# Kernel tuning notes

Hardware: AMD Instinct MI355X
Metric: run time of the kernel (lower is better)

Reference implementation:

```python
import jax, jax.numpy as jnp
import numpy as np
from jax import lax

H = 16  # hidden size

def lstm_dir(x_tbd, Wih, Whh, bih, bhh):
    # x_tbd: [T, B, D] -> outputs [T, B, H], final h [B, H]
    T, B, _ = x_tbd.shape
    xg = jnp.einsum('tbd,gd->tbg', x_tbd, Wih) + bih + bhh  # [T, B, 4H]
    def step(carry, xt):
        h, c = carry
        g = xt + h @ Whh.T
        i, f, gg, o = jnp.split(g, 4, axis=-1)  # PyTorch gate order i,f,g,o
        i = jax.nn.sigmoid(i); f = jax.nn.sigmoid(f)
        gg = jnp.tanh(gg); o = jax.nn.sigmoid(o)
        c = f * c + i * gg
        h = o * jnp.tanh(c)
        return (h, c), h
    init = (jnp.zeros((B, H), x_tbd.dtype), jnp.zeros((B, H), x_tbd.dtype))
    (hT, cT), hs = lax.scan(step, init, xg)
    return hs, hT

def bi_layer(x_tbd, pf, pb):
    hs_f, hT_f = lstm_dir(x_tbd, *pf)
    hs_b_rev, hT_b = lstm_dir(x_tbd[::-1], *pb)
    out = jnp.concatenate([hs_f, hs_b_rev[::-1]], axis=-1)  # [T, B, 2H]
    return out, hT_f, hT_b


def setup_inputs() -> dict:
    key = jax.random.key(0)
    ks = iter(jax.random.split(key, 32))
    B, T = 4096, 512
    d = {"x": jax.random.normal(next(ks), (B, T), jnp.float32)}
    def w(shape):
        return jax.random.normal(next(ks), shape, jnp.float32) * 0.2
    # layer 0 (input dim 1), forward / backward directions
    for s in ('f', 'b'):
        d[f'Wih0{s}'] = w((4 * H, 1)); d[f'Whh0{s}'] = w((4 * H, H))
        d[f'bih0{s}'] = jnp.zeros((4 * H,), jnp.float32)
        d[f'bhh0{s}'] = jnp.zeros((4 * H,), jnp.float32)
    # layer 1 (input dim 2H = 32)
    for s in ('f', 'b'):
        d[f'Wih1{s}'] = w((4 * H, 2 * H)); d[f'Whh1{s}'] = w((4 * H, H))
        d[f'bih1{s}'] = jnp.zeros((4 * H,), jnp.float32)
        d[f'bhh1{s}'] = jnp.zeros((4 * H,), jnp.float32)
    # MLP head: Linear(32,25), Linear(25,20)
    d['W1'] = w((25, 2 * H)); d['b1'] = jnp.zeros((25,), jnp.float32)
    d['W2'] = w((20, 25)); d['b2'] = jnp.zeros((20,), jnp.float32)
    return d


def reference(x, Wih0f, Whh0f, bih0f, bhh0f, Wih0b, Whh0b, bih0b, bhh0b,
              Wih1f, Whh1f, bih1f, bhh1f, Wih1b, Whh1b, bih1b, bhh1b,
              W1, b1, W2, b2):
    # x: [B, T] -> unsqueeze(2) -> [B, T, 1]; scan over time, so transpose to [T, B, 1]
    x_tbd = x.T[:, :, None]
    o0, _, _ = bi_layer(x_tbd, (Wih0f, Whh0f, bih0f, bhh0f), (Wih0b, Whh0b, bih0b, bhh0b))
    # dropout=0.1 between layers is inactive in eval mode (reference = eval)
    _, hT_f, hT_b = bi_layer(o0, (Wih1f, Whh1f, bih1f, bhh1f), (Wih1b, Whh1b, bih1b, bhh1b))
    # torch: cat((h[-1], h[-2]), 1) = (last-layer backward, last-layer forward)
    feat = jnp.concatenate([hT_b, hT_f], axis=1)  # [B, 32]
    z = jax.nn.elu(feat)
    z = jax.nn.elu(z @ W1.T + b1)
    z = jax.nn.elu(z @ W2.T + b2)
    return z  # [B, 20]
```

## Files before the change

### kernel.cpp

```cpp
#include <hip/hip_runtime.h>
#include <stdint.h>

#define TT 512
#define BB 4096
#define NT8 512
#define LOG2E 1.4426950408889634f

typedef _Float16 half8_t __attribute__((ext_vector_type(8)));
typedef __fp16 fp16x2_t __attribute__((ext_vector_type(2)));
typedef float f32x4 __attribute__((ext_vector_type(4)));
typedef float f32x2 __attribute__((ext_vector_type(2)));

union FragU { uint4 u4; half8_t h8; };
union PkU { fp16x2_t h2; unsigned int u; };

__device__ __forceinline__ float rcp_(float x){ return __builtin_amdgcn_rcpf(x); }
__device__ __forceinline__ float exp2_(float x){ return __builtin_amdgcn_exp2f(x); }
__device__ __forceinline__ float elu_(float x){ return x > 0.0f ? x : (exp2_(x * LOG2E) - 1.0f); }
__device__ __forceinline__ int mini_(int a, int b){ return a < b ? a : b; }
__device__ __forceinline__ float maskhi_(float x){ return __uint_as_float(__float_as_uint(x) & 0xFFFFE000u); }
__device__ __forceinline__ unsigned int pkrtz_(float a, float b){
    PkU p; p.h2 = __builtin_amdgcn_cvt_pkrtz(a, b); return p.u;
}
__device__ __forceinline__ unsigned int pkrne_(float a, float b){
    PkU p; p.h2[0] = (__fp16)a; p.h2[1] = (__fp16)b; return p.u;
}

__device__ __forceinline__ f32x4 MFMA(half8_t a, half8_t b, f32x4 c) {
    return __builtin_amdgcn_mfma_f32_16x16x32_f16(a, b, c, 0, 0, 0);
}

__device__ __forceinline__ f32x4 ld4_(const float* p){ return *(const f32x4*)p; }

__device__ __forceinline__ half8_t packA8s(const float* s, float sc) {
    half8_t h;
#pragma unroll
    for (int k = 0; k < 8; ++k) h[k] = (_Float16)(s[k] * sc);
    return h;
}
__device__ __forceinline__ half8_t zero8_() {
    half8_t h;
#pragma unroll
    for (int k = 0; k < 8; ++k) h[k] = (_Float16)0.0f;
    return h;
}

__device__ __forceinline__ void cell2p_(f32x2 gi, f32x2 gf, f32x2 gg, f32x2 go,
                                        f32x2& c, f32x2& h) {
    f32x2 ei, ef, eg, eo;
    ei[0] = exp2_(-gi[0]); ei[1] = exp2_(-gi[1]);
    ef[0] = exp2_(-gf[0]); ef[1] = exp2_(-gf[1]);
    eg[0] = exp2_(-gg[0]); eg[1] = exp2_(-gg[1]);
    eo[0] = exp2_(-go[0]); eo[1] = exp2_(-go[1]);
    const f32x2 one = {1.0f, 1.0f};
    f32x2 ai = one + ei, af = one + ef, ag = one + eg, ao = one + eo;
    f32x2 pif = ai * af, pgo = ag * ao;
    f32x2 P = pif * pgo;
    f32x2 R; R[0] = rcp_(P[0]); R[1] = rcp_(P[1]);
    f32x2 I = R * (af * pgo);
    f32x2 F = R * (ai * pgo);
    f32x2 Gt = R * (pif * ao);
    f32x2 O = R * (pif * ag);
    f32x2 G = Gt + Gt - one;
    c = F * c + I * G;
    f32x2 ct = c * (-2.0f * LOG2E);
    f32x2 et; et[0] = exp2_(ct[0]); et[1] = exp2_(ct[1]);
    f32x2 den = one + et;
    f32x2 Rt; Rt[0] = rcp_(den[0]); Rt[1] = rcp_(den[1]);
    f32x2 T = Rt + Rt - one;
    h = O * T;
}


struct PA {
    const float *x;
    const float *WihF, *WhhF, *bihF, *bhhF;
    const float *WihB, *WhhB, *bihB, *bhhB;
    char* ws;
};

__global__ __launch_bounds__(256) void phaseA_k(PA p) {
    const int tid = threadIdx.x;
    const int lane = tid & 63;
    const int wv   = tid >> 6;
    const int q = lane >> 4, b = lane & 15, c = b & 7;
    const bool hi8 = b >= 8;
    const int chain = blockIdx.x * 4 + wv;
    const int tile = chain >> 1, dir = chain & 1;

    const float* Wih = dir ? p.WihB : p.WihF;
    const float* Whh = dir ? p.WhhB : p.WhhF;
    const float* bih = dir ? p.bihB : p.bihF;
    const float* bhh = dir ? p.bhhB : p.bhhF;

    auto mkA = [&](int m, float sc)->half8_t {
        if (q < 2) return packA8s(Whh + (16*m + b)*16 + 8*q, sc);
        half8_t h = zero8_();
        if (q == 2) {
            float w = Wih[16*m + b] * sc;
            h[0] = (_Float16)w;
            h[1] = (_Float16)w;
        }
        return h;
    };
    half8_t A0 = mkA(0, LOG2E);
    half8_t A1 = mkA(1, LOG2E);
    half8_t A2 = mkA(2, 2.0f*LOG2E);
    half8_t A3 = mkA(3, LOG2E);

    f32x4 bias0 = (ld4_(bih +      4*q) + ld4_(bhh +      4*q)) * LOG2E;
    f32x4 bias1 = (ld4_(bih + 16 + 4*q) + ld4_(bhh + 16 + 4*q)) * LOG2E;
    f32x4 bias2 = (ld4_(bih + 32 + 4*q) + ld4_(bhh + 32 + 4*q)) * (2.0f*LOG2E);
    f32x4 bias3 = (ld4_(bih + 48 + 4*q) + ld4_(bhh + 48 + 4*q)) * LOG2E;

    const int uu = 4*q + (hi8 ? 2 : 0);
    const int sa0 = 32*(q&1) + c;
    const int sa1 = sa0 + 8;
    const int sa2 = sa0 + 16;
    const int sa3 = sa0 + 24;
    const bool qlt2 = q < 2;
    const bool q2   = q == 2;

    unsigned int hh = 0u;
    f32x2 cc = {0.f, 0.f};

    const char* xbase = (const char*)p.x + (size_t)tile*8*TT*4;
    const int   xoff  = c*TT*4;
    char*       wsbase = p.ws + (size_t)tile*TT*512;
    const int   woff  = c*64 + dir*32 + uu*2;

    auto xld = [&](int s_)->float {
        int s = mini_(s_, TT-1);
        int t = dir ? (TT-1-s) : s;
        return *(const float*)(xbase + (size_t)t*4 + xoff);
    };

    auto step = [&](float xv, int t) {
        float mh = maskhi_(xv);
        unsigned int xp = pkrtz_(mh, xv - mh);
        unsigned int s0 = (unsigned int)__shfl((int)hh, sa0);
        unsigned int s1 = (unsigned int)__shfl((int)hh, sa1);
        unsigned int s2 = (unsigned int)__shfl((int)hh, sa2);
        unsigned int s3 = (unsigned int)__shfl((int)hh, sa3);
        FragU hf;
        hf.u4.x = qlt2 ? s0 : (q2 ? xp : 0u);
        hf.u4.y = qlt2 ? s1 : 0u;
        hf.u4.z = qlt2 ? s2 : 0u;
        hf.u4.w = qlt2 ? s3 : 0u;
        f32x4 r0 = MFMA(A0, hf.h8, bias0);
        f32x4 r1 = MFMA(A1, hf.h8, bias1);
        f32x4 r2 = MFMA(A2, hf.h8, bias2);
        f32x4 r3 = MFMA(A3, hf.h8, bias3);
        f32x2 gi, gf, gg, go;
        gi[0] = hi8 ? r0[2] : r0[0]; gi[1] = hi8 ? r0[3] : r0[1];
        gf[0] = hi8 ? r1[2] : r1[0]; gf[1] = hi8 ? r1[3] : r1[1];
        gg[0] = hi8 ? r2[2] : r2[0]; gg[1] = hi8 ? r2[3] : r2[1];
        go[0] = hi8 ? r3[2] : r3[0]; go[1] = hi8 ? r3[3] : r3[1];
        f32x2 hv;
        cell2p_(gi, gf, gg, go, cc, hv);
        hh = pkrne_(hv[0], hv[1]);
        *(unsigned int*)(wsbase + (size_t)t*512 + woff) = hh;
    };

    float xv0 = xld(0), xv1 = xld(1), xv2 = xld(2), xv3 = xld(3);
    for (int s = 0; s < TT; s += 4) {
        const int t0 = dir ? (TT-1-s) : s;
        const int d  = dir ? -1 : 1;
        step(xv0, t0      ); xv0 = xld(s+4);
        step(xv1, t0 + d  ); xv1 = xld(s+5);
        step(xv2, t0 + 2*d); xv2 = xld(s+6);
        step(xv3, t0 + 3*d); xv3 = xld(s+7);
    }
}

struct PB {
    const float *WihF, *WhhF, *bihF, *bhhF;
    const float *WihB, *WhhB, *bihB, *bhhB;
    const char* ws;
    float* hT;
};

__global__ __launch_bounds__(256) void phaseB_k(PB p) {
    const int tid = threadIdx.x;
    const int lane = tid & 63;
    const int wv   = tid >> 6;
    const int q = lane >> 4, b = lane & 15, c = b & 7;
    const bool hi8 = b >= 8;
    const int chain = blockIdx.x * 4 + wv;
    const int tile = chain >> 1, dir = chain & 1;

    const float* Wih = dir ? p.WihB : p.WihF;
    const float* Whh = dir ? p.WhhB : p.WhhF;
    const float* bih = dir ? p.bihB : p.bihF;
    const float* bhh = dir ? p.bhhB : p.bhhF;

    const float SC0 = LOG2E, SC1 = LOG2E, SC2 = 2.0f*LOG2E, SC3 = LOG2E;

    half8_t wi0 = packA8s(Wih + (     b)*32 + 8*q, SC0);
    half8_t wi1 = packA8s(Wih + (16 + b)*32 + 8*q, SC1);
    half8_t wi2 = packA8s(Wih + (32 + b)*32 + 8*q, SC2);
    half8_t wi3 = packA8s(Wih + (48 + b)*32 + 8*q, SC3);

    half8_t wh0 = (q < 2) ? packA8s(Whh + (     b)*16 + 8*q, SC0) : zero8_();
    half8_t wh1 = (q < 2) ? packA8s(Whh + (16 + b)*16 + 8*q, SC1) : zero8_();
    half8_t wh2 = (q < 2) ? packA8s(Whh + (32 + b)*16 + 8*q, SC2) : zero8_();
    half8_t wh3 = (q < 2) ? packA8s(Whh + (48 + b)*16 + 8*q, SC3) : zero8_();

    f32x4 bias0 = (ld4_(bih +      4*q) + ld4_(bhh +      4*q)) * SC0;
    f32x4 bias1 = (ld4_(bih + 16 + 4*q) + ld4_(bhh + 16 + 4*q)) * SC1;
    f32x4 bias2 = (ld4_(bih + 32 + 4*q) + ld4_(bhh + 32 + 4*q)) * SC2;
    f32x4 bias3 = (ld4_(bih + 48 + 4*q) + ld4_(bhh + 48 + 4*q)) * SC3;

    const int uu = 4*q + (hi8 ? 2 : 0);
    const int sa0 = 32*(q&1) + c;
    const int sa1 = sa0 + 8;
    const int sa2 = sa0 + 16;
    const int sa3 = sa0 + 24;
    const bool qlt2 = q < 2;

    unsigned int hh = 0u;
    f32x2 cc = {0.f, 0.f};
    f32x2 hv = {0.f, 0.f};

    const char* wsbase = p.ws + (size_t)tile*TT*512;
    const int   xoff   = c*64 + q*16;

    auto xld = [&](int s_)->uint4 {
        int s = mini_(s_, TT-1);
        int t = dir ? (TT-1-s) : s;
        return *(const uint4*)(wsbase + (size_t)t*512 + xoff);
    };

    auto step = [&](uint4 xin) {
        FragU xf; xf.u4 = xin;
        unsigned int s0 = (unsigned int)__shfl((int)hh, sa0);
        unsigned int s1 = (unsigned int)__shfl((int)hh, sa1);
        unsigned int s2 = (unsigned int)__shfl((int)hh, sa2);
        unsigned int s3 = (unsigned int)__shfl((int)hh, sa3);
        FragU hf;
        hf.u4.x = qlt2 ? s0 : 0u;
        hf.u4.y = qlt2 ? s1 : 0u;
        hf.u4.z = qlt2 ? s2 : 0u;
        hf.u4.w = qlt2 ? s3 : 0u;
        f32x4 r0 = MFMA(wi0, xf.h8, bias0);
        f32x4 r1 = MFMA(wi1, xf.h8, bias1);
        f32x4 r2 = MFMA(wi2, xf.h8, bias2);
        f32x4 r3 = MFMA(wi3, xf.h8, bias3);
        r0 = MFMA(wh0, hf.h8, r0);
        r1 = MFMA(wh1, hf.h8, r1);
        r2 = MFMA(wh2, hf.h8, r2);
        r3 = MFMA(wh3, hf.h8, r3);
        f32x2 gi, gf, gg, go;
        gi[0] = hi8 ? r0[2] : r0[0]; gi[1] = hi8 ? r0[3] : r0[1];
        gf[0] = hi8 ? r1[2] : r1[0]; gf[1] = hi8 ? r1[3] : r1[1];
        gg[0] = hi8 ? r2[2] : r2[0]; gg[1] = hi8 ? r2[3] : r2[1];
        go[0] = hi8 ? r3[2] : r3[0]; go[1] = hi8 ? r3[3] : r3[1];
        cell2p_(gi, gf, gg, go, cc, hv);
        hh = pkrne_(hv[0], hv[1]);
    };

    uint4 xb0 = xld(0), xb1 = xld(1), xb2 = xld(2), xb3 = xld(3);
    for (int s = 0; s < TT; s += 4) {
        step(xb0); xb0 = xld(s+4);
        step(xb1); xb1 = xld(s+5);
        step(xb2); xb2 = xld(s+6);
        step(xb3); xb3 = xld(s+7);
    }

    const int batch = tile*8 + c;
    float* hp = p.hT + ((size_t)(dir ? BB : 0) + batch)*16 + uu;
    float2 ho; ho.x = hv[0]; ho.y = hv[1];
    *(float2*)hp = ho;
}

struct PC {
    const float* hT;
    const float *W1, *b1, *W2, *b2;
    float* out;
};

__global__ __launch_bounds__(64) void head_k(PC p) {
    const int B = blockIdx.x * 64 + threadIdx.x;
    const float* hf = p.hT + (size_t)B*16;
    const float* hb = p.hT + ((size_t)BB + B)*16;

    float z0[32];
#pragma unroll
    for (int k = 0; k < 16; ++k) z0[k] = elu_(hb[k]);
#pragma unroll
    for (int k = 0; k < 16; ++k) z0[16+k] = elu_(hf[k]);

    float z1[25];
#pragma unroll
    for (int o = 0; o < 25; ++o) {
        float a = p.b1[o];
#pragma unroll
        for (int k = 0; k < 32; ++k) a = fmaf(p.W1[o*32 + k], z0[k], a);
        z1[o] = elu_(a);
    }
#pragma unroll
    for (int o = 0; o < 20; ++o) {
        float a = p.b2[o];
#pragma unroll
        for (int k = 0; k < 25; ++k) a = fmaf(p.W2[o*25 + k], z1[k], a);
        p.out[(size_t)B*20 + o] = elu_(a);
    }
}

extern "C" void kernel_launch(void* const* d_in, const int* in_sizes, int n_in,
                              void* d_out, int out_size, void* d_ws, size_t ws_size,
                              hipStream_t stream) {
    (void)in_sizes; (void)n_in; (void)out_size;

    const size_t frag_bytes = (size_t)NT8 * TT * 512;
    const size_t hT_bytes   = (size_t)2 * BB * 16 * sizeof(float);
    size_t hT_off = (ws_size >= frag_bytes + hT_bytes) ? frag_bytes
                                                       : (ws_size - hT_bytes);
    char* ws = (char*)d_ws;
    float* hT = (float*)(ws + hT_off);

    PA pa;
    pa.x = (const float*)d_in[0];
    pa.WihF = (const float*)d_in[1];  pa.WhhF = (const float*)d_in[2];
    pa.bihF = (const float*)d_in[3];  pa.bhhF = (const float*)d_in[4];
    pa.WihB = (const float*)d_in[5];  pa.WhhB = (const float*)d_in[6];
    pa.bihB = (const float*)d_in[7];  pa.bhhB = (const float*)d_in[8];
    pa.ws = ws;
    hipLaunchKernelGGL(phaseA_k, dim3(256), dim3(256), 0, stream, pa);

    PB pb;
    pb.WihF = (const float*)d_in[9];   pb.WhhF = (const float*)d_in[10];
    pb.bihF = (const float*)d_in[11];  pb.bhhF = (const float*)d_in[12];
    pb.WihB = (const float*)d_in[13];  pb.WhhB = (const float*)d_in[14];
    pb.bihB = (const float*)d_in[15];  pb.bhhB = (const float*)d_in[16];
    pb.ws = ws; pb.hT = hT;
    hipLaunchKernelGGL(phaseB_k, dim3(256), dim3(256), 0, stream, pb);

    PC pc;
    pc.hT = hT;
    pc.W1 = (const float*)d_in[17]; pc.b1 = (const float*)d_in[18];
    pc.W2 = (const float*)d_in[19]; pc.b2 = (const float*)d_in[20];
    pc.out = (float*)d_out;
    hipLaunchKernelGGL(head_k, dim3(BB/64), dim3(64), 0, stream, pc);
}
```

Before: 306.3 us.

## Software-pipeline input MFMAs and exchange hidden state through LDS

In the layer-1 recurrence, the input-projection MFMAs for the next timestep now run ahead of the recurrent MFMAs for the current one, so they sit off the serial dependency chain. The four cross-lane shuffles that rebuilt the h fragment each step are replaced by one 32-bit LDS store, a wave barrier, and one 128-bit LDS read. The aim is a shorter critical path per timestep. The cost is more live accumulator registers and an LDS round-trip latency in each step.

```diff
diff --git a/kernel.cpp b/kernel.cpp
--- a/kernel.cpp
+++ b/kernel.cpp
@@ -181,9 +181,11 @@
 };
 
 __global__ __launch_bounds__(256) void phaseB_k(PB p) {
+    __shared__ uint4 ldsAll[4 * 16];
     const int tid = threadIdx.x;
     const int lane = tid & 63;
     const int wv   = tid >> 6;
+    char* lds = (char*)ldsAll + wv * 256;
     const int q = lane >> 4, b = lane & 15, c = b & 7;
     const bool hi8 = b >= 8;
     const int chain = blockIdx.x * 4 + wv;
@@ -211,14 +213,13 @@
     f32x4 bias2 = (ld4_(bih + 32 + 4*q) + ld4_(bhh + 32 + 4*q)) * SC2;
     f32x4 bias3 = (ld4_(bih + 48 + 4*q) + ld4_(bhh + 48 + 4*q)) * SC3;
 
-    const int uu = 4*q + (hi8 ? 2 : 0);
-    const int sa0 = 32*(q&1) + c;
-    const int sa1 = sa0 + 8;
-    const int sa2 = sa0 + 16;
-    const int sa3 = sa0 + 24;
-    const bool qlt2 = q < 2;
-
-    unsigned int hh = 0u;
+    const int uu  = 4*q + (hi8 ? 2 : 0);
+    const int who = c*32 + uu*2;
+    const int rdo = c*32 + (q&1)*16;
+
+    ((unsigned int*)lds)[lane & 63] = 0u;
+    __builtin_amdgcn_wave_barrier();
+
     f32x2 cc = {0.f, 0.f};
     f32x2 hv = {0.f, 0.f};
 
@@ -231,40 +232,47 @@
         return *(const uint4*)(wsbase + (size_t)t*512 + xoff);
     };
 
-    auto step = [&](uint4 xin) {
+    auto wiM = [&](uint4 xin, f32x4& o0, f32x4& o1, f32x4& o2, f32x4& o3) {
         FragU xf; xf.u4 = xin;
-        unsigned int s0 = (unsigned int)__shfl((int)hh, sa0);
-        unsigned int s1 = (unsigned int)__shfl((int)hh, sa1);
-        unsigned int s2 = (unsigned int)__shfl((int)hh, sa2);
-        unsigned int s3 = (unsigned int)__shfl((int)hh, sa3);
-        FragU hf;
-        hf.u4.x = qlt2 ? s0 : 0u;
-        hf.u4.y = qlt2 ? s1 : 0u;
-        hf.u4.z = qlt2 ? s2 : 0u;
-        hf.u4.w = qlt2 ? s3 : 0u;
-        f32x4 r0 = MFMA(wi0, xf.h8, bias0);
-        f32x4 r1 = MFMA(wi1, xf.h8, bias1);
-        f32x4 r2 = MFMA(wi2, xf.h8, bias2);
-        f32x4 r3 = MFMA(wi3, xf.h8, bias3);
-        r0 = MFMA(wh0, hf.h8, r0);
-        r1 = MFMA(wh1, hf.h8, r1);
-        r2 = MFMA(wh2, hf.h8, r2);
-        r3 = MFMA(wh3, hf.h8, r3);
+        o0 = MFMA(wi0, xf.h8, bias0);
+        o1 = MFMA(wi1, xf.h8, bias1);
+        o2 = MFMA(wi2, xf.h8, bias2);
+        o3 = MFMA(wi3, xf.h8, bias3);
+    };
+
+    auto stepWh = [&](f32x4 p0, f32x4 p1, f32x4 p2, f32x4 p3) {
+        FragU hf; hf.u4 = *(const uint4*)(lds + rdo);
+        f32x4 r0 = MFMA(wh0, hf.h8, p0);
+        f32x4 r1 = MFMA(wh1, hf.h8, p1);
+        f32x4 r2 = MFMA(wh2, hf.h8, p2);
+        f32x4 r3 = MFMA(wh3, hf.h8, p3);
         f32x2 gi, gf, gg, go;
         gi[0] = hi8 ? r0[2] : r0[0]; gi[1] = hi8 ? r0[3] : r0[1];
         gf[0] = hi8 ? r1[2] : r1[0]; gf[1] = hi8 ? r1[3] : r1[1];
         gg[0] = hi8 ? r2[2] : r2[0]; gg[1] = hi8 ? r2[3] : r2[1];
         go[0] = hi8 ? r3[2] : r3[0]; go[1] = hi8 ? r3[3] : r3[1];
         cell2p_(gi, gf, gg, go, cc, hv);
-        hh = pkrne_(hv[0], hv[1]);
+        unsigned int hh = pkrne_(hv[0], hv[1]);
+        *(unsigned int*)(lds + who) = hh;
+        __builtin_amdgcn_wave_barrier();
     };
 
     uint4 xb0 = xld(0), xb1 = xld(1), xb2 = xld(2), xb3 = xld(3);
+    f32x4 pa0, pa1, pa2, pa3, pb0, pb1, pb2, pb3;
+    wiM(xb0, pa0, pa1, pa2, pa3);
     for (int s = 0; s < TT; s += 4) {
-        step(xb0); xb0 = xld(s+4);
-        step(xb1); xb1 = xld(s+5);
-        step(xb2); xb2 = xld(s+6);
-        step(xb3); xb3 = xld(s+7);
+        wiM(xb1, pb0, pb1, pb2, pb3);
+        stepWh(pa0, pa1, pa2, pa3);
+        xb0 = xld(s+4);
+        wiM(xb2, pa0, pa1, pa2, pa3);
+        stepWh(pb0, pb1, pb2, pb3);
+        xb1 = xld(s+5);
+        wiM(xb3, pb0, pb1, pb2, pb3);
+        stepWh(pa0, pa1, pa2, pa3);
+        xb2 = xld(s+6);
+        wiM(xb0, pa0, pa1, pa2, pa3);
+        stepWh(pb0, pb1, pb2, pb3);
+        xb3 = xld(s+7);
     }
 
     const int batch = tile*8 + c;
```

New measurement: 286.7 us. 6.4% less time.
